# Optimization experiments

Measured on AMD Instinct MI355X. Metric: run time of the kernel, lower is better.

Reference implementation:

```python
import jax, jax.numpy as jnp
import numpy as np

N, E, D_IN, D_OUT = 50000, 300000, 256, 256
BN_EPS = 1e-5


def ccorr(a, b):
    # circular correlation: irfft(conj(rfft(a)) * rfft(b))
    return jnp.fft.irfft(jnp.conj(jnp.fft.rfft(a, axis=-1)) * jnp.fft.rfft(b, axis=-1), n=a.shape[-1], axis=-1)


def setup_inputs() -> dict:
    key = jax.random.key(0)
    ks = jax.random.split(key, 8)
    return {
        "node_ft": jax.random.normal(ks[0], (N, D_IN), dtype=jnp.float32),
        "edge_ft": jax.random.normal(ks[1], (E, D_IN), dtype=jnp.float32),
        "norm": jax.random.uniform(ks[2], (N, 1), dtype=jnp.float32),
        "w_loop": jax.random.normal(ks[3], (D_IN, D_OUT), dtype=jnp.float32) * (1.414 / np.sqrt(D_IN)),
        "w_in": jax.random.normal(ks[4], (D_IN, D_OUT), dtype=jnp.float32) * (1.414 / np.sqrt(D_IN)),
        "loop_rel": jax.random.normal(ks[5], (1, D_IN), dtype=jnp.float32),
        "w_bias": jnp.zeros((D_OUT,), dtype=jnp.float32),
        "bn_gamma": jnp.ones((D_OUT,), dtype=jnp.float32),
        "bn_beta": jnp.zeros((D_OUT,), dtype=jnp.float32),
        "src": jax.random.randint(ks[6], (E,), 0, N, dtype=jnp.int32),
        "dst": jax.random.randint(ks[7], (E,), 0, N, dtype=jnp.int32),
    }


def reference(node_ft, edge_ft, norm, w_loop, w_in, loop_rel, w_bias, bn_gamma, bn_beta, src, dst):
    n_nodes = node_ft.shape[0]
    # self-loop message: ccorr(ft, loop_rel) @ w_loop  [N, d_out]
    loop_msg = ccorr(node_ft, loop_rel) @ w_loop
    # per-edge message: ccorr(src_ft, edge_ft) @ w_in  [E, d_out]
    msg = ccorr(node_ft[src], edge_ft) @ w_in
    # scatter-sum aggregation then norm multiply (apply_func)
    agg = jax.ops.segment_sum(msg, dst, num_segments=n_nodes) * norm
    h = agg + w_bias + loop_msg
    # BatchNorm1d (training mode: batch stats, biased variance)
    mean = jnp.mean(h, axis=0)
    var = jnp.var(h, axis=0)
    h = (h - mean) * jax.lax.rsqrt(var + BN_EPS) * bn_gamma + bn_beta
    return jnp.tanh(h)
```

## Files before the change

### kernel.cpp

```cpp
#include <hip/hip_runtime.h>
#include <hip/hip_bf16.h>

#define NN 50000
#define EE 300000
#define BN_EPS 1e-5f
#define NFW 288
#define TWOPI_256 0.024543692606170259f

typedef __attribute__((ext_vector_type(8))) _Float16 half8;
typedef __attribute__((ext_vector_type(2))) _Float16 half2v;
typedef __attribute__((ext_vector_type(4))) float f32x4;
#define MFMA16F __builtin_amdgcn_mfma_f32_16x16x32_f16

__device__ __align__(16) _Float16 g_NF[(size_t)NN * NFW];
__device__ __align__(16) _Float16 g_MSG[(size_t)EE * 256];
__device__ float g_Wle[256 * 256];
__device__ __align__(16) unsigned short g_FB[8 * 20 * 64 * 8];
__device__ __align__(16) unsigned short g_CB[9 * 16 * 64 * 8];
__device__ __align__(16) unsigned short g_WLEB[8 * 16 * 64 * 8];
__device__ int g_hist[NN];
__device__ int g_off[NN + 1];
__device__ int g_cursor[NN];
__device__ int g_pos[EE];
__device__ int g_bsum[128];
__device__ int g_bbase[128];

__device__ __forceinline__ void atomAddF(float* p, float v) { unsafeAtomicAdd(p, v); }

__device__ __forceinline__ unsigned short f2hu(float x) {
    union { _Float16 f; unsigned short u; } c;
    c.f = (_Float16)x;
    return c.u;
}

__device__ __forceinline__ void stage_write(char* A, const float4* stg, int t) {
#pragma unroll
    for (int q = 0; q < 8; ++q) {
        int idx = q * 512 + t;
        int row = idx >> 6, c4 = idx & 63;
        union { _Float16 f[4]; ushort4 u; } r;
        r.f[0] = (_Float16)stg[q].x; r.f[1] = (_Float16)stg[q].y;
        r.f[2] = (_Float16)stg[q].z; r.f[3] = (_Float16)stg[q].w;
        int ks = c4 >> 3;
        int off = ((row >> 4) * 8 + ks) * 1024 +
                  ((((((c4 >> 1) & 3) << 4) | (row & 15)) * 16) ^ (ks << 4)) +
                  (c4 & 1) * 8;
        *(ushort4*)(A + off) = r.u;
    }
}

__global__ __launch_bounds__(512) void hist_kernel(const int* __restrict__ dst, int E) {
    int e = blockIdx.x * 512 + threadIdx.x;
    if (e < E) atomicAdd(&g_hist[dst[e]], 1);
}

__global__ __launch_bounds__(512) void scanA_kernel(int N) {
    __shared__ int arr[512];
    int t = threadIdx.x, b = blockIdx.x * 512 + t;
    int cnt = (b < N) ? g_hist[b] : 0;
    arr[t] = cnt;
    __syncthreads();
#pragma unroll
    for (int off = 1; off < 512; off <<= 1) {
        int v = (t >= off) ? arr[t - off] : 0;
        __syncthreads();
        arr[t] += v;
        __syncthreads();
    }
    if (b < N) g_off[b] = arr[t] - cnt;
    if (t == 511) g_bsum[blockIdx.x] = arr[511];
}

__global__ __launch_bounds__(128) void scanB_kernel(int nblk) {
    __shared__ int arr[128];
    int t = threadIdx.x;
    int v0 = (t < nblk) ? g_bsum[t] : 0;
    arr[t] = v0;
    __syncthreads();
#pragma unroll
    for (int off = 1; off < 128; off <<= 1) {
        int v = (t >= off) ? arr[t - off] : 0;
        __syncthreads();
        arr[t] += v;
        __syncthreads();
    }
    if (t < nblk) g_bbase[t] = arr[t] - v0;
}

__global__ __launch_bounds__(512) void scanC_kernel(int N) {
    int b = blockIdx.x * 512 + threadIdx.x;
    if (b < N) {
        int v = g_off[b] + g_bbase[blockIdx.x];
        g_off[b] = v;
        g_cursor[b] = v;
        if (b == N - 1) g_off[N] = v + g_hist[b];
    }
}

__global__ __launch_bounds__(512) void pos_kernel(const int* __restrict__ dst, int E) {
    int e = blockIdx.x * 512 + threadIdx.x;
    if (e < E) {
        int pos = atomicAdd(&g_cursor[dst[e]], 1);
        g_pos[e] = pos;
    }
}

__global__ __launch_bounds__(256) void wle_kernel(
    const float* __restrict__ loop_rel, const float* __restrict__ w_loop,
    float* __restrict__ W_le) {
    __shared__ float lr[256];
    const int d = threadIdx.x, j = blockIdx.x;
    lr[d] = loop_rel[d];
    __syncthreads();
    float acc = 0.f;
#pragma unroll 4
    for (int k = 0; k < 256; ++k)
        acc = fmaf(lr[(j + k) & 255], w_loop[k * 256 + d], acc);
    W_le[j * 256 + d] = acc;
}

__global__ __launch_bounds__(512) void fb_pack() {
    int b = blockIdx.x, ks = b / 20, nt = b % 20;
    int t = threadIdx.x, lane = t >> 3, e = t & 7;
    int k = 32 * ks + 8 * (lane >> 4) + e;
    int r2 = nt * 16 + (lane & 15);
    float val = 0.f;
    if (r2 < 258) {
        int f = r2 >> 1;
        int m = (f * k) & 255;
        float s, c;
        sincosf((float)m * TWOPI_256, &s, &c);
        val = (r2 & 1) ? -s : c;
    }
    g_FB[((ks * 20 + nt) * 64 + lane) * 8 + e] = f2hu(val);
}

__global__ __launch_bounds__(512) void cb_pack(const float* __restrict__ w_in) {
    __shared__ float ct[256], st[256];
    int t = threadIdx.x;
    if (t < 256) {
        float s, c;
        sincosf((float)t * TWOPI_256, &s, &c);
        ct[t] = c; st[t] = s;
    }
    __syncthreads();
    int b = blockIdx.x, ks = b / 16, nt = b % 16;
    int lane = t >> 3, e = t & 7;
    int kk = 32 * ks + 8 * (lane >> 4) + e;
    int d = nt * 16 + (lane & 15);
    float val = 0.f;
    if (kk < 258) {
        int f = kk >> 1;
        float cf = (f == 0 || f == 128) ? (1.f / 256.f) : (2.f / 256.f);
        const float* tab = (kk & 1) ? st : ct;
        float sgn = (kk & 1) ? -1.f : 1.f;
        float acc = 0.f;
        for (int k = 0; k < 256; ++k)
            acc = fmaf(tab[(f * k) & 255], w_in[k * 256 + d], acc);
        val = cf * sgn * acc;
    }
    g_CB[((ks * 16 + nt) * 64 + lane) * 8 + e] = f2hu(val);
}

__global__ __launch_bounds__(512) void wleb_pack() {
    int b = blockIdx.x, ks = b / 16, nt = b % 16;
    int t = threadIdx.x, lane = t >> 3, e = t & 7;
    int k = 32 * ks + 8 * (lane >> 4) + e;
    int d = nt * 16 + (lane & 15);
    g_WLEB[((ks * 16 + nt) * 64 + lane) * 8 + e] = f2hu(g_Wle[k * 256 + d]);
}

__global__ __launch_bounds__(512, 4) void nfloop_kernel(
    const float* __restrict__ node_ft, const float* __restrict__ w_bias,
    float* __restrict__ out, int N) {
    __shared__ char smem[32768];
    unsigned short* A = (unsigned short*)smem;
    const int t = threadIdx.x;
    const long long r0 = (long long)blockIdx.x * 64;
    {
        float4 stg[8];
#pragma unroll
        for (int q = 0; q < 8; ++q) {
            int idx = q * 512 + t;
            long long gr = r0 + (idx >> 6);
            if (gr >= N) gr = N - 1;
            stg[q] = ((const float4*)node_ft)[gr * 64 + (idx & 63)];
        }
        stage_write(smem, stg, t);
    }
    __syncthreads();

    const int lane = t & 63, w = t >> 6;
    const int mw = w >> 2, nw = w & 3;
    const int l15 = lane & 15, lg = lane >> 4;

    {
        f32x4 acc[2][5] = {};
#pragma unroll
        for (int ks = 0; ks < 8; ++ks) {
            half8 a0 = *(const half8*)((char*)A + ((2 * mw + 0) * 8 + ks) * 1024 + ((lane * 16) ^ (ks << 4)));
            half8 a1 = *(const half8*)((char*)A + ((2 * mw + 1) * 8 + ks) * 1024 + ((lane * 16) ^ (ks << 4)));
#pragma unroll
            for (int j = 0; j < 4; ++j) {
                int tn = nw + 4 * j;
                half8 bf = *(const half8*)(g_FB + ((size_t)(ks * 20 + tn) * 64 + lane) * 8);
                acc[0][j] = MFMA16F(a0, bf, acc[0][j], 0, 0, 0);
                acc[1][j] = MFMA16F(a1, bf, acc[1][j], 0, 0, 0);
            }
            if (nw == 0) {
                half8 bf = *(const half8*)(g_FB + ((size_t)(ks * 20 + 16) * 64 + lane) * 8);
                acc[0][4] = MFMA16F(a0, bf, acc[0][4], 0, 0, 0);
                acc[1][4] = MFMA16F(a1, bf, acc[1][4], 0, 0, 0);
            }
        }
#pragma unroll
        for (int mt = 0; mt < 2; ++mt)
#pragma unroll
            for (int j = 0; j < 5; ++j) {
                int tn = nw + 4 * j;
                if (tn > 16 || (j == 4 && nw != 0)) continue;
                int r2 = tn * 16 + l15;
#pragma unroll
                for (int r = 0; r < 4; ++r) {
                    long long gr = r0 + (2 * mw + mt) * 16 + lg * 4 + r;
                    if (gr < N && r2 < 258)
                        g_NF[gr * NFW + r2] = (_Float16)acc[mt][j][r];
                }
            }
    }
    {
        f32x4 acc[2][4] = {};
#pragma unroll
        for (int ks = 0; ks < 8; ++ks) {
            half8 a0 = *(const half8*)((char*)A + ((2 * mw + 0) * 8 + ks) * 1024 + ((lane * 16) ^ (ks << 4)));
            half8 a1 = *(const half8*)((char*)A + ((2 * mw + 1) * 8 + ks) * 1024 + ((lane * 16) ^ (ks << 4)));
#pragma unroll
            for (int j = 0; j < 4; ++j) {
                half8 bf = *(const half8*)(g_WLEB + ((size_t)(ks * 16 + 4 * nw + j) * 64 + lane) * 8);
                acc[0][j] = MFMA16F(a0, bf, acc[0][j], 0, 0, 0);
                acc[1][j] = MFMA16F(a1, bf, acc[1][j], 0, 0, 0);
            }
        }
#pragma unroll
        for (int j = 0; j < 4; ++j) {
            const int col = (4 * nw + j) * 16 + l15;
            const float bj = w_bias[col];
#pragma unroll
            for (int mt = 0; mt < 2; ++mt)
#pragma unroll
                for (int r = 0; r < 4; ++r) {
                    long long gr = r0 + (2 * mw + mt) * 16 + lg * 4 + r;
                    if (gr < N)
                        out[gr * 256 + col] = acc[mt][j][r] + bj;
                }
        }
    }
}

__global__ __launch_bounds__(512, 4) void edgeA_kernel(
    const float* __restrict__ edge_ft, const int* __restrict__ src, int E) {
    __shared__ char smem[36864];
    unsigned short* A = (unsigned short*)smem;
    unsigned short* Z = (unsigned short*)smem;

    const int t = threadIdx.x;
    const long long ebase = (long long)blockIdx.x * 64;
    const int lane = t & 63, w = t >> 6;
    const int mw = w >> 2, nw = w & 3;
    const int l15 = lane & 15, lg = lane >> 4;
    const bool odd = (l15 & 1);

    int srcv[2][4], posv[2][4];
#pragma unroll
    for (int mt = 0; mt < 2; ++mt)
#pragma unroll
        for (int r = 0; r < 4; ++r) {
            long long ge = ebase + (2 * mw + mt) * 16 + lg * 4 + r;
            if (ge >= E) ge = E - 1;
            srcv[mt][r] = src[ge];
            posv[mt][r] = g_pos[ge];
        }

    {
        float4 stg[8];
#pragma unroll
        for (int q = 0; q < 8; ++q) {
            long long ge = ebase + q * 8 + (t >> 6);
            if (ge >= E) ge = E - 1;
            stg[q] = ((const float4*)edge_ft)[ge * 64 + (t & 63)];
        }
        stage_write(smem, stg, t);
    }
    __syncthreads();

    f32x4 acc1[2][5] = {};
#pragma unroll
    for (int ks = 0; ks < 8; ++ks) {
        half8 a0 = *(const half8*)((char*)A + ((2 * mw + 0) * 8 + ks) * 1024 + ((lane * 16) ^ (ks << 4)));
        half8 a1 = *(const half8*)((char*)A + ((2 * mw + 1) * 8 + ks) * 1024 + ((lane * 16) ^ (ks << 4)));
#pragma unroll
        for (int j = 0; j < 4; ++j) {
            int tn = nw + 4 * j;
            half8 bf = *(const half8*)(g_FB + ((size_t)(ks * 20 + tn) * 64 + lane) * 8);
            acc1[0][j] = MFMA16F(a0, bf, acc1[0][j], 0, 0, 0);
            acc1[1][j] = MFMA16F(a1, bf, acc1[1][j], 0, 0, 0);
        }
        if (nw == 0) {
            half8 bf = *(const half8*)(g_FB + ((size_t)(ks * 20 + 16) * 64 + lane) * 8);
            acc1[0][4] = MFMA16F(a0, bf, acc1[0][4], 0, 0, 0);
            acc1[1][4] = MFMA16F(a1, bf, acc1[1][4], 0, 0, 0);
        }
    }
    __syncthreads();

#pragma unroll
    for (int mt = 0; mt < 2; ++mt) {
        int tm = 2 * mw + mt;
#pragma unroll
        for (int j = 0; j < 5; ++j) {
            int tn = nw + 4 * j;
            if (tn >= 18) continue;
            int r2 = tn * 16 + l15;
#pragma unroll
            for (int r = 0; r < 4; ++r) {
                int e = tm * 16 + lg * 4 + r;
                float z = 0.f;
                if (r2 < 258) {
                    float own = acc1[mt][j][r];
                    float oth = __shfl_xor(own, 1);
                    union { unsigned int u; half2v h; } cv;
                    cv.u = *(const unsigned int*)(g_NF +
                        (long long)srcv[mt][r] * NFW + (r2 & ~1));
                    float br = (float)cv.h[0], bi = (float)cv.h[1];
                    z = odd ? (br * own - bi * oth) : (br * own + bi * oth);
                }
                int ksz = r2 >> 5;
                int off = ((e >> 4) * 9 + ksz) * 1024 +
                          ((((((r2 >> 3) & 3) << 4) | (e & 15)) * 16) ^ (ksz << 4)) +
                          (r2 & 7) * 2;
                *(unsigned short*)((char*)Z + off) = f2hu(z);
            }
        }
    }
    __syncthreads();

    f32x4 acc2[2][4] = {};
#pragma unroll
    for (int ks = 0; ks < 9; ++ks) {
        half8 a0 = *(const half8*)((char*)Z + ((2 * mw + 0) * 9 + ks) * 1024 + ((lane * 16) ^ (ks << 4)));
        half8 a1 = *(const half8*)((char*)Z + ((2 * mw + 1) * 9 + ks) * 1024 + ((lane * 16) ^ (ks << 4)));
#pragma unroll
        for (int j = 0; j < 4; ++j) {
            half8 bf = *(const half8*)(g_CB + ((size_t)(ks * 16 + 4 * nw + j) * 64 + lane) * 8);
            acc2[0][j] = MFMA16F(a0, bf, acc2[0][j], 0, 0, 0);
            acc2[1][j] = MFMA16F(a1, bf, acc2[1][j], 0, 0, 0);
        }
    }

#pragma unroll
    for (int mt = 0; mt < 2; ++mt)
#pragma unroll
        for (int r = 0; r < 4; ++r) {
            long long ge = ebase + (2 * mw + mt) * 16 + lg * 4 + r;
            if (ge < E) {
                _Float16* mrow = g_MSG + (size_t)posv[mt][r] * 256;
#pragma unroll
                for (int j = 0; j < 4; ++j)
                    mrow[(4 * nw + j) * 16 + l15] = (_Float16)acc2[mt][j][r];
            }
        }
}

__global__ __launch_bounds__(512) void reduceB_kernel(
    const float* __restrict__ norm, float* __restrict__ out,
    float* __restrict__ s1g, float* __restrict__ s2g, int N) {
    __shared__ float s1l[256], s2l[256];
    const int t = threadIdx.x;
    if (t < 256) { s1l[t] = 0.f; s2l[t] = 0.f; }
    __syncthreads();
    const int w = t >> 6, lane = t & 63;
    float a1[4] = {0.f, 0.f, 0.f, 0.f}, a2[4] = {0.f, 0.f, 0.f, 0.f};

#pragma unroll 1
    for (int i = 0; i < 8; ++i) {
        int n = blockIdx.x * 64 + w * 8 + i;
        if (n >= N) break;
        const int s = g_off[n], e2 = g_off[n + 1];
        const float nrm = norm[n];
        float4 ms = make_float4(0.f, 0.f, 0.f, 0.f);
        int i2 = s;
        for (; i2 + 1 < e2; i2 += 2) {
            half2v p0 = *(const half2v*)(g_MSG + (size_t)i2 * 256 + lane * 4);
            half2v p1 = *(const half2v*)(g_MSG + (size_t)i2 * 256 + lane * 4 + 2);
            half2v q0 = *(const half2v*)(g_MSG + (size_t)(i2 + 1) * 256 + lane * 4);
            half2v q1 = *(const half2v*)(g_MSG + (size_t)(i2 + 1) * 256 + lane * 4 + 2);
            ms.x += (float)p0[0] + (float)q0[0];
            ms.y += (float)p0[1] + (float)q0[1];
            ms.z += (float)p1[0] + (float)q1[0];
            ms.w += (float)p1[1] + (float)q1[1];
        }
        if (i2 < e2) {
            half2v p0 = *(const half2v*)(g_MSG + (size_t)i2 * 256 + lane * 4);
            half2v p1 = *(const half2v*)(g_MSG + (size_t)i2 * 256 + lane * 4 + 2);
            ms.x += (float)p0[0]; ms.y += (float)p0[1];
            ms.z += (float)p1[0]; ms.w += (float)p1[1];
        }
        float4 hv = ((const float4*)out)[(size_t)n * 64 + lane];
        hv.x = fmaf(ms.x, nrm, hv.x);
        hv.y = fmaf(ms.y, nrm, hv.y);
        hv.z = fmaf(ms.z, nrm, hv.z);
        hv.w = fmaf(ms.w, nrm, hv.w);
        ((float4*)out)[(size_t)n * 64 + lane] = hv;
        a1[0] += hv.x; a2[0] += hv.x * hv.x;
        a1[1] += hv.y; a2[1] += hv.y * hv.y;
        a1[2] += hv.z; a2[2] += hv.z * hv.z;
        a1[3] += hv.w; a2[3] += hv.w * hv.w;
    }
#pragma unroll
    for (int c = 0; c < 4; ++c) {
        atomicAdd(&s1l[lane * 4 + c], a1[c]);
        atomicAdd(&s2l[lane * 4 + c], a2[c]);
    }
    __syncthreads();
    if (t < 256) {
        atomAddF(&s1g[t], s1l[t]);
        atomAddF(&s2g[t], s2l[t]);
    }
}

__global__ __launch_bounds__(256) void finalize_kernel(
    float* __restrict__ out, const float* __restrict__ s1g,
    const float* __restrict__ s2g, const float* __restrict__ gamma,
    const float* __restrict__ beta, int N) {
    long long i4 = (long long)blockIdx.x * blockDim.x + threadIdx.x;
    long long tot = (long long)N * 64;
    if (i4 >= tot) return;
    const int dg = (int)(i4 & 63);
    float4 h = ((float4*)out)[i4];
    const float4 s1 = ((const float4*)s1g)[dg];
    const float4 s2 = ((const float4*)s2g)[dg];
    const float4 g = ((const float4*)gamma)[dg];
    const float4 b = ((const float4*)beta)[dg];
    const float invN = 1.f / (float)N;
    float4 o;
    { float m = s1.x * invN; float v = s2.x * invN - m * m;
      o.x = tanhf(fmaf(h.x - m, rsqrtf(v + BN_EPS) * g.x, b.x)); }
    { float m = s1.y * invN; float v = s2.y * invN - m * m;
      o.y = tanhf(fmaf(h.y - m, rsqrtf(v + BN_EPS) * g.y, b.y)); }
    { float m = s1.z * invN; float v = s2.z * invN - m * m;
      o.z = tanhf(fmaf(h.z - m, rsqrtf(v + BN_EPS) * g.z, b.z)); }
    { float m = s1.w * invN; float v = s2.w * invN - m * m;
      o.w = tanhf(fmaf(h.w - m, rsqrtf(v + BN_EPS) * g.w, b.w)); }
    ((float4*)out)[i4] = o;
}

extern "C" void kernel_launch(void* const* d_in, const int* in_sizes, int n_in,
                              void* d_out, int out_size, void* d_ws, size_t ws_size,
                              hipStream_t stream) {
    const float* node_ft  = (const float*)d_in[0];
    const float* edge_ft  = (const float*)d_in[1];
    const float* norm     = (const float*)d_in[2];
    const float* w_loop   = (const float*)d_in[3];
    const float* w_in     = (const float*)d_in[4];
    const float* loop_rel = (const float*)d_in[5];
    const float* w_bias   = (const float*)d_in[6];
    const float* bn_gamma = (const float*)d_in[7];
    const float* bn_beta  = (const float*)d_in[8];
    const int*   src      = (const int*)d_in[9];
    const int*   dst      = (const int*)d_in[10];

    const int N = in_sizes[2];
    const int E = in_sizes[9];
    float* out = (float*)d_out;

    float* s1g = (float*)d_ws;
    float* s2g = s1g + 256;

    hipMemsetAsync(d_ws, 0, 512 * sizeof(float), stream);

    float* Wle_ptr = nullptr;
    hipGetSymbolAddress((void**)&Wle_ptr, HIP_SYMBOL(g_Wle));
    void* hist_ptr = nullptr;
    hipGetSymbolAddress(&hist_ptr, HIP_SYMBOL(g_hist));
    hipMemsetAsync(hist_ptr, 0, (size_t)N * sizeof(int), stream);

    const int sblk = (N + 511) / 512;
    const int eblk = (E + 511) / 512;

    hist_kernel<<<eblk, 512, 0, stream>>>(dst, E);
    scanA_kernel<<<sblk, 512, 0, stream>>>(N);
    scanB_kernel<<<1, 128, 0, stream>>>(sblk);
    scanC_kernel<<<sblk, 512, 0, stream>>>(N);
    pos_kernel<<<eblk, 512, 0, stream>>>(dst, E);

    wle_kernel<<<256, 256, 0, stream>>>(loop_rel, w_loop, Wle_ptr);
    fb_pack<<<8 * 20, 512, 0, stream>>>();
    cb_pack<<<9 * 16, 512, 0, stream>>>(w_in);
    wleb_pack<<<8 * 16, 512, 0, stream>>>();

    nfloop_kernel<<<(N + 63) / 64, 512, 0, stream>>>(node_ft, w_bias, out, N);
    edgeA_kernel<<<(E + 63) / 64, 512, 0, stream>>>(edge_ft, src, E);
    reduceB_kernel<<<(N + 63) / 64, 512, 0, stream>>>(norm, out, s1g, s2g, N);
    finalize_kernel<<<(int)(((long long)N * 64 + 255) / 256), 256, 0, stream>>>(
        out, s1g, s2g, bn_gamma, bn_beta, N);
}
```

Measured before the change: 475.1 us.

## Aggregate frequency-domain products per node before the w_in GEMM

The per-edge products are no longer multiplied by the combined inverse-FFT/w_in matrix. They are written as 288-wide fp16 rows to a dst-sorted buffer, summed per destination node, scaled by norm, and then put through one GEMM per node block inside a new reduceZ kernel. This relies on the linearity of the matmul and removes the E-row GEMM and the Z shared-memory staging from the edge kernel. A second counting sort by src is added so the edge kernel reads node features in src order, in exchange for extra launches and atomics. The intermediate buffer grows from 256 to 288 halves per edge, which adds write and read traffic.

Result: slower. 583.7 us (+22.8%).

```diff
diff --git a/kernel.cpp b/kernel.cpp
--- a/kernel.cpp
+++ b/kernel.cpp
@@ -8,22 +8,24 @@
 #define TWOPI_256 0.024543692606170259f
 
 typedef __attribute__((ext_vector_type(8))) _Float16 half8;
+typedef __attribute__((ext_vector_type(4))) _Float16 half4v;
 typedef __attribute__((ext_vector_type(2))) _Float16 half2v;
 typedef __attribute__((ext_vector_type(4))) float f32x4;
 #define MFMA16F __builtin_amdgcn_mfma_f32_16x16x32_f16
 
 __device__ __align__(16) _Float16 g_NF[(size_t)NN * NFW];
-__device__ __align__(16) _Float16 g_MSG[(size_t)EE * 256];
+__device__ __align__(16) _Float16 g_ZS[(size_t)EE * NFW];
 __device__ float g_Wle[256 * 256];
 __device__ __align__(16) unsigned short g_FB[8 * 20 * 64 * 8];
 __device__ __align__(16) unsigned short g_CB[9 * 16 * 64 * 8];
 __device__ __align__(16) unsigned short g_WLEB[8 * 16 * 64 * 8];
-__device__ int g_hist[NN];
-__device__ int g_off[NN + 1];
-__device__ int g_cursor[NN];
+__device__ int g_histD[NN], g_offD[NN + 1], g_curD[NN];
+__device__ int g_histS[NN], g_offS[NN], g_curS[NN];
 __device__ int g_pos[EE];
-__device__ int g_bsum[128];
-__device__ int g_bbase[128];
+__device__ int g_eidx[EE];
+__device__ int g_esrc[EE];
+__device__ int g_epos[EE];
+__device__ int g_bsum[128], g_bbase[128];
 
 __device__ __forceinline__ void atomAddF(float* p, float v) { unsafeAtomicAdd(p, v); }
 
@@ -49,25 +51,27 @@
     }
 }
 
-__global__ __launch_bounds__(512) void hist_kernel(const int* __restrict__ dst, int E) {
+__global__ __launch_bounds__(512) void histK(const int* __restrict__ key,
+                                             int* __restrict__ hist, int E) {
     int e = blockIdx.x * 512 + threadIdx.x;
-    if (e < E) atomicAdd(&g_hist[dst[e]], 1);
-}
-
-__global__ __launch_bounds__(512) void scanA_kernel(int N) {
+    if (e < E) atomicAdd(&hist[key[e]], 1);
+}
+
+__global__ __launch_bounds__(512) void scanA_kernel(const int* __restrict__ cnt,
+                                                    int* __restrict__ off, int N) {
     __shared__ int arr[512];
     int t = threadIdx.x, b = blockIdx.x * 512 + t;
-    int cnt = (b < N) ? g_hist[b] : 0;
-    arr[t] = cnt;
-    __syncthreads();
-#pragma unroll
-    for (int off = 1; off < 512; off <<= 1) {
-        int v = (t >= off) ? arr[t - off] : 0;
+    int c = (b < N) ? cnt[b] : 0;
+    arr[t] = c;
+    __syncthreads();
+#pragma unroll
+    for (int o = 1; o < 512; o <<= 1) {
+        int v = (t >= o) ? arr[t - o] : 0;
         __syncthreads();
         arr[t] += v;
         __syncthreads();
     }
-    if (b < N) g_off[b] = arr[t] - cnt;
+    if (b < N) off[b] = arr[t] - c;
     if (t == 511) g_bsum[blockIdx.x] = arr[511];
 }
 
@@ -78,8 +82,8 @@
     arr[t] = v0;
     __syncthreads();
 #pragma unroll
-    for (int off = 1; off < 128; off <<= 1) {
-        int v = (t >= off) ? arr[t - off] : 0;
+    for (int o = 1; o < 128; o <<= 1) {
+        int v = (t >= o) ? arr[t - o] : 0;
         __syncthreads();
         arr[t] += v;
         __syncthreads();
@@ -87,21 +91,32 @@
     if (t < nblk) g_bbase[t] = arr[t] - v0;
 }
 
-__global__ __launch_bounds__(512) void scanC_kernel(int N) {
+__global__ __launch_bounds__(512) void scanC_kernel(int* __restrict__ off,
+                                                    int* __restrict__ cursor,
+                                                    const int* __restrict__ cnt,
+                                                    int N, int writeTotal) {
     int b = blockIdx.x * 512 + threadIdx.x;
     if (b < N) {
-        int v = g_off[b] + g_bbase[blockIdx.x];
-        g_off[b] = v;
-        g_cursor[b] = v;
-        if (b == N - 1) g_off[N] = v + g_hist[b];
-    }
-}
-
-__global__ __launch_bounds__(512) void pos_kernel(const int* __restrict__ dst, int E) {
+        int v = off[b] + g_bbase[blockIdx.x];
+        off[b] = v;
+        cursor[b] = v;
+        if (writeTotal && b == N - 1) off[N] = v + cnt[b];
+    }
+}
+
+__global__ __launch_bounds__(512) void posD_kernel(const int* __restrict__ dst, int E) {
+    int e = blockIdx.x * 512 + threadIdx.x;
+    if (e < E) g_pos[e] = atomicAdd(&g_curD[dst[e]], 1);
+}
+
+__global__ __launch_bounds__(512) void posS_kernel(const int* __restrict__ src, int E) {
     int e = blockIdx.x * 512 + threadIdx.x;
     if (e < E) {
-        int pos = atomicAdd(&g_cursor[dst[e]], 1);
-        g_pos[e] = pos;
+        int s = src[e];
+        int p = atomicAdd(&g_curS[s], 1);
+        g_eidx[p] = e;
+        g_esrc[p] = s;
+        g_epos[p] = g_pos[e];
     }
 }
 
@@ -258,10 +273,9 @@
 }
 
 __global__ __launch_bounds__(512, 4) void edgeA_kernel(
-    const float* __restrict__ edge_ft, const int* __restrict__ src, int E) {
-    __shared__ char smem[36864];
+    const float* __restrict__ edge_ft, int E) {
+    __shared__ char smem[32768];
     unsigned short* A = (unsigned short*)smem;
-    unsigned short* Z = (unsigned short*)smem;
 
     const int t = threadIdx.x;
     const long long ebase = (long long)blockIdx.x * 64;
@@ -277,8 +291,8 @@
         for (int r = 0; r < 4; ++r) {
             long long ge = ebase + (2 * mw + mt) * 16 + lg * 4 + r;
             if (ge >= E) ge = E - 1;
-            srcv[mt][r] = src[ge];
-            posv[mt][r] = g_pos[ge];
+            srcv[mt][r] = g_esrc[ge];
+            posv[mt][r] = g_epos[ge];
         }
 
     {
@@ -287,7 +301,7 @@
         for (int q = 0; q < 8; ++q) {
             long long ge = ebase + q * 8 + (t >> 6);
             if (ge >= E) ge = E - 1;
-            stg[q] = ((const float4*)edge_ft)[ge * 64 + (t & 63)];
+            stg[q] = ((const float4*)edge_ft)[(long long)g_eidx[ge] * 64 + (t & 63)];
         }
         stage_write(smem, stg, t);
     }
@@ -311,35 +325,94 @@
             acc1[1][4] = MFMA16F(a1, bf, acc1[1][4], 0, 0, 0);
         }
     }
-    __syncthreads();
 
 #pragma unroll
     for (int mt = 0; mt < 2; ++mt) {
-        int tm = 2 * mw + mt;
 #pragma unroll
         for (int j = 0; j < 5; ++j) {
             int tn = nw + 4 * j;
-            if (tn >= 18) continue;
+            if (tn >= 17) continue;
             int r2 = tn * 16 + l15;
 #pragma unroll
             for (int r = 0; r < 4; ++r) {
-                int e = tm * 16 + lg * 4 + r;
+                float own = acc1[mt][j][r];
+                float oth = __shfl_xor(own, 1);
                 float z = 0.f;
                 if (r2 < 258) {
-                    float own = acc1[mt][j][r];
-                    float oth = __shfl_xor(own, 1);
                     union { unsigned int u; half2v h; } cv;
                     cv.u = *(const unsigned int*)(g_NF +
                         (long long)srcv[mt][r] * NFW + (r2 & ~1));
                     float br = (float)cv.h[0], bi = (float)cv.h[1];
                     z = odd ? (br * own - bi * oth) : (br * own + bi * oth);
                 }
-                int ksz = r2 >> 5;
-                int off = ((e >> 4) * 9 + ksz) * 1024 +
-                          ((((((r2 >> 3) & 3) << 4) | (e & 15)) * 16) ^ (ksz << 4)) +
-                          (r2 & 7) * 2;
-                *(unsigned short*)((char*)Z + off) = f2hu(z);
-            }
+                float zo = __shfl_xor(z, 1);
+                if (!odd && r2 < 258) {
+                    union { half2v h; unsigned int u; } pk;
+                    pk.h[0] = (_Float16)z; pk.h[1] = (_Float16)zo;
+                    *(unsigned int*)(g_ZS + (size_t)posv[mt][r] * NFW + r2) = pk.u;
+                }
+            }
+        }
+    }
+}
+
+__global__ __launch_bounds__(512) void reduceZ_kernel(
+    const float* __restrict__ norm, float* __restrict__ out,
+    float* __restrict__ s1g, float* __restrict__ s2g, int N) {
+    __shared__ char A[36864];
+    __shared__ float s1l[256], s2l[256];
+    const int t = threadIdx.x;
+    const int lane = t & 63, w = t >> 6;
+    const int mw = w >> 2, nw = w & 3;
+    const int l15 = lane & 15, lg = lane >> 4;
+
+    {
+        int4 zero = make_int4(0, 0, 0, 0);
+#pragma unroll
+        for (int q = 0; q < 5; ++q) {
+            int i = q * 512 + t;
+            if (i < 2304) ((int4*)A)[i] = zero;
+        }
+        if (t < 256) { s1l[t] = 0.f; s2l[t] = 0.f; }
+    }
+    __syncthreads();
+
+#pragma unroll 1
+    for (int i = 0; i < 8; ++i) {
+        int n = blockIdx.x * 64 + w * 8 + i;
+        if (n >= N) break;
+        const int s = g_offD[n], e2 = g_offD[n + 1];
+        float4 zs = make_float4(0.f, 0.f, 0.f, 0.f);
+        float zt0 = 0.f, zt1 = 0.f;
+        for (int i2 = s; i2 < e2; ++i2) {
+            const _Float16* zr = g_ZS + (size_t)i2 * NFW;
+            half4v v = *(const half4v*)(zr + 4 * lane);
+            zs.x += (float)v[0]; zs.y += (float)v[1];
+            zs.z += (float)v[2]; zs.w += (float)v[3];
+            if (lane == 0) {
+                half2v tv = *(const half2v*)(zr + 256);
+                zt0 += (float)tv[0]; zt1 += (float)tv[1];
+            }
+        }
+        const float nrm = norm[n];
+        const int row = w * 8 + i;
+        {
+            union { _Float16 f[4]; ushort4 u; } pk;
+            pk.f[0] = (_Float16)(zs.x * nrm); pk.f[1] = (_Float16)(zs.y * nrm);
+            pk.f[2] = (_Float16)(zs.z * nrm); pk.f[3] = (_Float16)(zs.w * nrm);
+            int c4 = lane, ks = c4 >> 3;
+            int off = ((row >> 4) * 9 + ks) * 1024 +
+                      ((((((c4 >> 1) & 3) << 4) | (row & 15)) * 16) ^ (ks << 4)) +
+                      (c4 & 1) * 8;
+            *(ushort4*)(A + off) = pk.u;
+        }
+        if (lane == 0) {
+            union { _Float16 f[4]; ushort4 u; } pk;
+            pk.f[0] = (_Float16)(zt0 * nrm); pk.f[1] = (_Float16)(zt1 * nrm);
+            pk.f[2] = (_Float16)0.f; pk.f[3] = (_Float16)0.f;
+            int off = ((row >> 4) * 9 + 8) * 1024 +
+                      (((row & 15) * 16) ^ (8 << 4));
+            *(ushort4*)(A + off) = pk.u;
         }
     }
     __syncthreads();
@@ -347,8 +420,8 @@
     f32x4 acc2[2][4] = {};
 #pragma unroll
     for (int ks = 0; ks < 9; ++ks) {
-        half8 a0 = *(const half8*)((char*)Z + ((2 * mw + 0) * 9 + ks) * 1024 + ((lane * 16) ^ (ks << 4)));
-        half8 a1 = *(const half8*)((char*)Z + ((2 * mw + 1) * 9 + ks) * 1024 + ((lane * 16) ^ (ks << 4)));
+        half8 a0 = *(const half8*)(A + ((2 * mw + 0) * 9 + ks) * 1024 + ((lane * 16) ^ (ks << 4)));
+        half8 a1 = *(const half8*)(A + ((2 * mw + 1) * 9 + ks) * 1024 + ((lane * 16) ^ (ks << 4)));
 #pragma unroll
         for (int j = 0; j < 4; ++j) {
             half8 bf = *(const half8*)(g_CB + ((size_t)(ks * 16 + 4 * nw + j) * 64 + lane) * 8);
@@ -357,69 +430,28 @@
         }
     }
 
+    float a1s[4] = {0.f, 0.f, 0.f, 0.f}, a2s[4] = {0.f, 0.f, 0.f, 0.f};
 #pragma unroll
     for (int mt = 0; mt < 2; ++mt)
 #pragma unroll
         for (int r = 0; r < 4; ++r) {
-            long long ge = ebase + (2 * mw + mt) * 16 + lg * 4 + r;
-            if (ge < E) {
-                _Float16* mrow = g_MSG + (size_t)posv[mt][r] * 256;
-#pragma unroll
-                for (int j = 0; j < 4; ++j)
-                    mrow[(4 * nw + j) * 16 + l15] = (_Float16)acc2[mt][j][r];
-            }
-        }
-}
-
-__global__ __launch_bounds__(512) void reduceB_kernel(
-    const float* __restrict__ norm, float* __restrict__ out,
-    float* __restrict__ s1g, float* __restrict__ s2g, int N) {
-    __shared__ float s1l[256], s2l[256];
-    const int t = threadIdx.x;
-    if (t < 256) { s1l[t] = 0.f; s2l[t] = 0.f; }
-    __syncthreads();
-    const int w = t >> 6, lane = t & 63;
-    float a1[4] = {0.f, 0.f, 0.f, 0.f}, a2[4] = {0.f, 0.f, 0.f, 0.f};
-
-#pragma unroll 1
-    for (int i = 0; i < 8; ++i) {
-        int n = blockIdx.x * 64 + w * 8 + i;
-        if (n >= N) break;
-        const int s = g_off[n], e2 = g_off[n + 1];
-        const float nrm = norm[n];
-        float4 ms = make_float4(0.f, 0.f, 0.f, 0.f);
-        int i2 = s;
-        for (; i2 + 1 < e2; i2 += 2) {
-            half2v p0 = *(const half2v*)(g_MSG + (size_t)i2 * 256 + lane * 4);
-            half2v p1 = *(const half2v*)(g_MSG + (size_t)i2 * 256 + lane * 4 + 2);
-            half2v q0 = *(const half2v*)(g_MSG + (size_t)(i2 + 1) * 256 + lane * 4);
-            half2v q1 = *(const half2v*)(g_MSG + (size_t)(i2 + 1) * 256 + lane * 4 + 2);
-            ms.x += (float)p0[0] + (float)q0[0];
-            ms.y += (float)p0[1] + (float)q0[1];
-            ms.z += (float)p1[0] + (float)q1[0];
-            ms.w += (float)p1[1] + (float)q1[1];
-        }
-        if (i2 < e2) {
-            half2v p0 = *(const half2v*)(g_MSG + (size_t)i2 * 256 + lane * 4);
-            half2v p1 = *(const half2v*)(g_MSG + (size_t)i2 * 256 + lane * 4 + 2);
-            ms.x += (float)p0[0]; ms.y += (float)p0[1];
-            ms.z += (float)p1[0]; ms.w += (float)p1[1];
-        }
-        float4 hv = ((const float4*)out)[(size_t)n * 64 + lane];
-        hv.x = fmaf(ms.x, nrm, hv.x);
-        hv.y = fmaf(ms.y, nrm, hv.y);
-        hv.z = fmaf(ms.z, nrm, hv.z);
-        hv.w = fmaf(ms.w, nrm, hv.w);
-        ((float4*)out)[(size_t)n * 64 + lane] = hv;
-        a1[0] += hv.x; a2[0] += hv.x * hv.x;
-        a1[1] += hv.y; a2[1] += hv.y * hv.y;
-        a1[2] += hv.z; a2[2] += hv.z * hv.z;
-        a1[3] += hv.w; a2[3] += hv.w * hv.w;
-    }
-#pragma unroll
-    for (int c = 0; c < 4; ++c) {
-        atomicAdd(&s1l[lane * 4 + c], a1[c]);
-        atomicAdd(&s2l[lane * 4 + c], a2[c]);
+            int rl = (2 * mw + mt) * 16 + lg * 4 + r;
+            long long n = (long long)blockIdx.x * 64 + rl;
+            if (n < N) {
+#pragma unroll
+                for (int j = 0; j < 4; ++j) {
+                    int col = (4 * nw + j) * 16 + l15;
+                    float h = out[n * 256 + col] + acc2[mt][j][r];
+                    out[n * 256 + col] = h;
+                    a1s[j] += h; a2s[j] += h * h;
+                }
+            }
+        }
+#pragma unroll
+    for (int j = 0; j < 4; ++j) {
+        int col = (4 * nw + j) * 16 + l15;
+        atomicAdd(&s1l[col], a1s[j]);
+        atomicAdd(&s2l[col], a2s[j]);
     }
     __syncthreads();
     if (t < 256) {
@@ -480,18 +512,30 @@
 
     float* Wle_ptr = nullptr;
     hipGetSymbolAddress((void**)&Wle_ptr, HIP_SYMBOL(g_Wle));
-    void* hist_ptr = nullptr;
-    hipGetSymbolAddress(&hist_ptr, HIP_SYMBOL(g_hist));
-    hipMemsetAsync(hist_ptr, 0, (size_t)N * sizeof(int), stream);
+    void *histD_ptr = nullptr, *histS_ptr = nullptr;
+    int *offD = nullptr, *offS = nullptr, *curD = nullptr, *curS = nullptr;
+    hipGetSymbolAddress(&histD_ptr, HIP_SYMBOL(g_histD));
+    hipGetSymbolAddress(&histS_ptr, HIP_SYMBOL(g_histS));
+    hipGetSymbolAddress((void**)&offD, HIP_SYMBOL(g_offD));
+    hipGetSymbolAddress((void**)&offS, HIP_SYMBOL(g_offS));
+    hipGetSymbolAddress((void**)&curD, HIP_SYMBOL(g_curD));
+    hipGetSymbolAddress((void**)&curS, HIP_SYMBOL(g_curS));
+    hipMemsetAsync(histD_ptr, 0, (size_t)N * sizeof(int), stream);
+    hipMemsetAsync(histS_ptr, 0, (size_t)N * sizeof(int), stream);
 
     const int sblk = (N + 511) / 512;
     const int eblk = (E + 511) / 512;
 
-    hist_kernel<<<eblk, 512, 0, stream>>>(dst, E);
-    scanA_kernel<<<sblk, 512, 0, stream>>>(N);
+    histK<<<eblk, 512, 0, stream>>>(dst, (int*)histD_ptr, E);
+    scanA_kernel<<<sblk, 512, 0, stream>>>((int*)histD_ptr, offD, N);
     scanB_kernel<<<1, 128, 0, stream>>>(sblk);
-    scanC_kernel<<<sblk, 512, 0, stream>>>(N);
-    pos_kernel<<<eblk, 512, 0, stream>>>(dst, E);
+    scanC_kernel<<<sblk, 512, 0, stream>>>(offD, curD, (int*)histD_ptr, N, 1);
+    posD_kernel<<<eblk, 512, 0, stream>>>(dst, E);
+    histK<<<eblk, 512, 0, stream>>>(src, (int*)histS_ptr, E);
+    scanA_kernel<<<sblk, 512, 0, stream>>>((int*)histS_ptr, offS, N);
+    scanB_kernel<<<1, 128, 0, stream>>>(sblk);
+    scanC_kernel<<<sblk, 512, 0, stream>>>(offS, curS, (int*)histS_ptr, N, 0);
+    posS_kernel<<<eblk, 512, 0, stream>>>(src, E);
 
     wle_kernel<<<256, 256, 0, stream>>>(loop_rel, w_loop, Wle_ptr);
     fb_pack<<<8 * 20, 512, 0, stream>>>();
@@ -499,8 +543,8 @@
     wleb_pack<<<8 * 16, 512, 0, stream>>>();
 
     nfloop_kernel<<<(N + 63) / 64, 512, 0, stream>>>(node_ft, w_bias, out, N);
-    edgeA_kernel<<<(E + 63) / 64, 512, 0, stream>>>(edge_ft, src, E);
-    reduceB_kernel<<<(N + 63) / 64, 512, 0, stream>>>(norm, out, s1g, s2g, N);
+    edgeA_kernel<<<(E + 63) / 64, 512, 0, stream>>>(edge_ft, E);
+    reduceZ_kernel<<<(N + 63) / 64, 512, 0, stream>>>(norm, out, s1g, s2g, N);
     finalize_kernel<<<(int)(((long long)N * 64 + 255) / 256), 256, 0, stream>>>(
         out, s1g, s2g, bn_gamma, bn_beta, N);
 }
```
